# Optimization experiments

Hardware: AMD Instinct MI355X
Metric: run time of the kernel (lower is better)

Reference implementation:

```python
import jax, jax.numpy as jnp
import numpy as np
import math

N_GENES_TOTAL = 5000   # full gene table (fragments.n_genes)
N_CELLS_TOTAL = 10000  # full cell count (libsize buffer)
NBINS = 128            # spline components per gene
N_LATENT = 64
B = 256                # n_cells in minibatch
G = 2000               # genes_oi
NCUTS = 500_000


def setup_inputs() -> dict:
    key = jax.random.key(0)
    ks = jax.random.split(key, 12)
    latent = jax.random.normal(ks[0], (B, N_LATENT), jnp.float32)
    genes_oi = jax.random.randint(ks[1], (G,), 0, N_GENES_TOTAL)
    cells_oi = jax.random.randint(ks[2], (B,), 0, N_CELLS_TOTAL)
    cut_coordinates = jax.random.uniform(ks[3], (NCUTS,), jnp.float32)
    cut_local_cellxgene_ix = jax.random.randint(ks[4], (NCUTS,), 0, B * G)
    cut_local_gene_ix = jax.random.randint(ks[5], (NCUTS,), 0, G)
    local_cellxgene_ix = jax.random.randint(ks[6], (NCUTS,), 0, B * G)
    s = 1.0 / math.sqrt(N_LATENT)
    logit_weight = jax.random.uniform(ks[7], (N_GENES_TOTAL, N_LATENT, NBINS), jnp.float32, -s, s)
    rho_weight = jax.random.uniform(ks[8], (N_GENES_TOTAL, N_LATENT), jnp.float32, -s / 100.0, s / 100.0)
    rho_bias = jax.random.uniform(ks[9], (N_GENES_TOTAL,), jnp.float32, 1e-4, 1e-2)
    libsize = jax.random.randint(ks[10], (N_CELLS_TOTAL,), 1000, 20000)
    spline_heights = 0.01 * jax.random.normal(ks[11], (N_GENES_TOTAL, NBINS), jnp.float32)
    return {
        "latent": latent, "genes_oi": genes_oi, "cells_oi": cells_oi,
        "cut_coordinates": cut_coordinates,
        "cut_local_cellxgene_ix": cut_local_cellxgene_ix,
        "cut_local_gene_ix": cut_local_gene_ix,
        "local_cellxgene_ix": local_cellxgene_ix,
        "logit_weight": logit_weight, "rho_weight": rho_weight,
        "rho_bias": rho_bias, "libsize": libsize,
        "spline_heights": spline_heights,
        "n_cells": B, "n_genes": G,
    }


def reference(latent, genes_oi, cells_oi, cut_coordinates,
              cut_local_cellxgene_ix, cut_local_gene_ix, local_cellxgene_ix,
              logit_weight, rho_weight, rho_bias, libsize, spline_heights,
              n_cells, n_genes):
    # Decoder with n_layers=0: nn is identity
    lw = logit_weight[genes_oi]                     # [G, L, C]
    rw = rho_weight[genes_oi]                       # [G, L]
    mixture_delta = jnp.einsum('bl,glc->bgc', latent, lw)   # [B, G, C]
    rho_delta = latent @ rw.T                       # [B, G]

    # gather per-cut mixture deltas
    delta_flat = mixture_delta.reshape(n_cells * n_genes, -1)
    delta_cut = delta_flat[cut_local_cellxgene_ix]  # [Ncuts, C]

    # spline/mixture log-likelihood: per-gene histogram density with delta
    gene_heights = spline_heights[genes_oi]         # [G, C]
    h = gene_heights[cut_local_gene_ix] + delta_cut  # [Ncuts, C]
    logp_bins = jax.nn.log_softmax(h, axis=-1)
    nbins = h.shape[-1]
    bin_ix = jnp.clip((cut_coordinates * nbins).astype(jnp.int32), 0, nbins - 1)
    likelihood_mixture = (
        jnp.take_along_axis(logp_bins, bin_ix[:, None], axis=-1)[:, 0]
        + jnp.log(jnp.float32(nbins))
    )

    # Poisson fragment-count likelihood
    rate = (rho_bias[genes_oi][None, :] * jnp.exp(rho_delta)
            * libsize[cells_oi].astype(jnp.float32)[:, None])   # [B, G]
    counts = jnp.bincount(local_cellxgene_ix, length=n_cells * n_genes)
    counts = counts.reshape(n_cells, n_genes).astype(jnp.float32)
    ll_counts = counts * jnp.log(rate) - rate - jax.scipy.special.gammaln(counts + 1.0)

    likelihood = likelihood_mixture.sum() + ll_counts.sum()
    return -likelihood
```

## Files before the change

kernel.cpp:

```cpp
#include <hip/hip_runtime.h>

#define LDIM 64
#define CDIM 128
#define NREP 8
#define SUBCAP 48
#define MAXPER (NREP * SUBCAP)
#define LOG128 4.8520302639196171f

typedef __attribute__((ext_vector_type(8))) short bfrag;
typedef __attribute__((ext_vector_type(4))) float f32x4;

static __device__ __forceinline__ unsigned short f2bf(float f) {
    unsigned int x = __float_as_uint(f);
    unsigned int r = (x + 0x7fffu + ((x >> 16) & 1u)) >> 16;
    return (unsigned short)r;
}
static __device__ __forceinline__ float bf2f(unsigned int u) {
    return __uint_as_float(u << 16);
}

__global__ __launch_bounds__(256) void zero_kernel(uint4* __restrict__ p, size_t n16,
                                                   float* __restrict__ out, int out_size) {
    size_t i = (size_t)blockIdx.x * blockDim.x + threadIdx.x;
    size_t stride = (size_t)gridDim.x * blockDim.x;
    for (; i < n16; i += stride) p[i] = make_uint4(0u, 0u, 0u, 0u);
    if (blockIdx.x == 0 && threadIdx.x < (unsigned)out_size) out[threadIdx.x] = 0.f;
}

__global__ __launch_bounds__(256) void prep1_kernel(
    const float* __restrict__ heights, unsigned short* __restrict__ hbf, int nheights,
    const float* __restrict__ latent, unsigned short* __restrict__ latbf, int nlat,
    const int* __restrict__ cut_pair, const int* __restrict__ cut_gene,
    const float* __restrict__ coord, const int* __restrict__ genes_oi,
    const int* __restrict__ local_cxg, unsigned int* __restrict__ cnt_rep,
    unsigned int* __restrict__ bucket, unsigned int* __restrict__ countsT,
    int ncuts, int B, int G, int N, unsigned int magicG) {
    int stride = gridDim.x * blockDim.x;
    int rep = blockIdx.x & (NREP - 1);
    int nb = 2 * G;
    for (int i = blockIdx.x * blockDim.x + threadIdx.x; i < N; i += stride) {
        if (i < nheights) hbf[i] = f2bf(heights[i]);
        if (i < nlat) latbf[i] = f2bf(latent[i]);
        if (i < ncuts) {
            unsigned int p = (unsigned int)cut_pair[i];
            unsigned int cell = __umulhi(p, magicG);
            unsigned int g = p - cell * (unsigned int)G;
            unsigned int gg = (unsigned int)genes_oi[cut_gene[i]];
            int bin = (int)(coord[i] * 128.0f);
            bin = min(max(bin, 0), 127);
            unsigned int bidx = g * 2u + (cell >> 7);
            unsigned int slot = atomicAdd(&cnt_rep[rep * nb + (int)bidx], 1u);
            if (slot < SUBCAP)
                bucket[(size_t)bidx * MAXPER + rep * SUBCAP + slot] =
                    (cell << 24) | (gg << 7) | (unsigned int)bin;
            unsigned int q = (unsigned int)local_cxg[i];
            unsigned int cell2 = __umulhi(q, magicG);
            unsigned int g2 = q - cell2 * (unsigned int)G;
            atomicAdd(&countsT[(size_t)g2 * (unsigned int)B + cell2], 1u);
        }
    }
}

__global__ __launch_bounds__(512, 6) void fused_kernel(
    const float* __restrict__ latent, const unsigned short* __restrict__ latbf,
    const int* __restrict__ genes_oi, const float* __restrict__ logit_weight,
    const unsigned short* __restrict__ hbf, const unsigned int* __restrict__ bucket,
    const unsigned int* __restrict__ cnt_rep, const unsigned int* __restrict__ countsT,
    const int* __restrict__ cells_oi,
    const float* __restrict__ rho_weight, const float* __restrict__ rho_bias,
    const int* __restrict__ libsize, int B, int G, float* __restrict__ out) {
    __shared__ unsigned short dlds[128 * CDIM];
    __shared__ unsigned short blds[CDIM * LDIM];
    __shared__ unsigned int clds[MAXPER];
    __shared__ unsigned int csum[NREP + 1];
    __shared__ float red[8];
    int t = threadIdx.x;
    int bid = blockIdx.x;
    int g = bid >> 1, half = bid & 1;
    int gene = genes_oi[g];
    int nb = 2 * G;

    {
        int n = t & 127;
        int k0 = (t >> 7) * 16;
        const float* src = logit_weight + (size_t)gene * LDIM * CDIM;
        float v[16];
        #pragma unroll
        for (int j = 0; j < 16; ++j) v[j] = src[(size_t)(k0 + j) * CDIM + n];
        #pragma unroll
        for (int h = 0; h < 2; ++h) {
            union { unsigned short u[8]; uint4 q; } pk;
            #pragma unroll
            for (int j = 0; j < 8; ++j) pk.u[j] = f2bf(v[h * 8 + j]);
            int kk = k0 + h * 8;
            *(uint4*)(blds + n * LDIM + (kk ^ ((n & 7) * 8))) = pk.q;
        }
    }
    if (t < NREP) csum[t + 1] = min(cnt_rep[t * nb + bid], (unsigned)SUBCAP);
    __syncthreads();

    int wv = t >> 6, ln = t & 63;
    int l15 = ln & 15, l4 = ln >> 4;
    f32x4 acc[8];
    #pragma unroll
    for (int n = 0; n < 8; ++n) acc[n] = (f32x4){0.f, 0.f, 0.f, 0.f};
    #pragma unroll
    for (int ks = 0; ks < 2; ++ks) {
        int kk = ks * 32 + l4 * 8;
        bfrag a = *(const bfrag*)(latbf + (half * 128 + wv * 16 + l15) * LDIM + kk);
        #pragma unroll
        for (int n = 0; n < 8; ++n) {
            int col = n * 16 + l15;
            bfrag b = *(const bfrag*)(blds + col * LDIM + (kk ^ ((col & 7) * 8)));
            acc[n] = __builtin_amdgcn_mfma_f32_16x16x32_bf16(a, b, acc[n], 0, 0, 0);
        }
    }
    #pragma unroll
    for (int n = 0; n < 8; ++n)
        #pragma unroll
        for (int r = 0; r < 4; ++r) {
            int row = wv * 16 + l4 * 4 + r;
            int col = n * 16 + l15;
            dlds[row * CDIM + (col ^ ((row & 7) * 8))] = f2bf(acc[n][r]);
        }
    if (t == 0) {
        csum[0] = 0;
        #pragma unroll
        for (int r = 0; r < NREP; ++r) csum[r + 1] += csum[r];
    }
    __syncthreads();

    {
        const unsigned int* bk = bucket + (size_t)bid * MAXPER;
        #pragma unroll
        for (int r = 0; r < NREP; ++r) {
            unsigned int base = csum[r], cr = csum[r + 1] - base;
            for (unsigned int i = (unsigned int)t; i < cr; i += 512u)
                clds[base + i] = bk[r * SUBCAP + i];
        }
    }
    __syncthreads();

    float accs = 0.f;
    {
        unsigned int C = csum[NREP];
        int grp = t >> 3, sub = t & 7;
        for (unsigned int i = (unsigned int)grp; i < C; i += 64u) {
            unsigned int rc = clds[i];
            int row = (int)((rc >> 24) & 127u);
            unsigned int gg = (rc >> 7) & 0x1FFFu;
            int sw = (row & 7) * 8;
            uint4 dva = *(const uint4*)(dlds + row * CDIM + ((sub * 16) ^ sw));
            uint4 dvb = *(const uint4*)(dlds + row * CDIM + ((sub * 16 + 8) ^ sw));
            const uint4* hp = (const uint4*)(hbf + ((size_t)gg << 7) + sub * 16);
            uint4 hva = hp[0], hvb = hp[1];
            float h0  = bf2f(hva.x & 0xffffu) + bf2f(dva.x & 0xffffu);
            float h1  = bf2f(hva.x >> 16)     + bf2f(dva.x >> 16);
            float h2  = bf2f(hva.y & 0xffffu) + bf2f(dva.y & 0xffffu);
            float h3  = bf2f(hva.y >> 16)     + bf2f(dva.y >> 16);
            float h4  = bf2f(hva.z & 0xffffu) + bf2f(dva.z & 0xffffu);
            float h5  = bf2f(hva.z >> 16)     + bf2f(dva.z >> 16);
            float h6  = bf2f(hva.w & 0xffffu) + bf2f(dva.w & 0xffffu);
            float h7  = bf2f(hva.w >> 16)     + bf2f(dva.w >> 16);
            float h8  = bf2f(hvb.x & 0xffffu) + bf2f(dvb.x & 0xffffu);
            float h9  = bf2f(hvb.x >> 16)     + bf2f(dvb.x >> 16);
            float h10 = bf2f(hvb.y & 0xffffu) + bf2f(dvb.y & 0xffffu);
            float h11 = bf2f(hvb.y >> 16)     + bf2f(dvb.y >> 16);
            float h12 = bf2f(hvb.z & 0xffffu) + bf2f(dvb.z & 0xffffu);
            float h13 = bf2f(hvb.z >> 16)     + bf2f(dvb.z >> 16);
            float h14 = bf2f(hvb.w & 0xffffu) + bf2f(dvb.w & 0xffffu);
            float h15 = bf2f(hvb.w >> 16)     + bf2f(dvb.w >> 16);
            float s = __expf(h0)  + __expf(h1)  + __expf(h2)  + __expf(h3)
                    + __expf(h4)  + __expf(h5)  + __expf(h6)  + __expf(h7)
                    + __expf(h8)  + __expf(h9)  + __expf(h10) + __expf(h11)
                    + __expf(h12) + __expf(h13) + __expf(h14) + __expf(h15);
            #pragma unroll
            for (int o = 1; o < 8; o <<= 1) s += __shfl_xor(s, o);
            int bin = (int)(rc & 127u);
            int e = bin & 15;
            float sel = h0;
            sel = (e == 1)  ? h1  : sel;
            sel = (e == 2)  ? h2  : sel;
            sel = (e == 3)  ? h3  : sel;
            sel = (e == 4)  ? h4  : sel;
            sel = (e == 5)  ? h5  : sel;
            sel = (e == 6)  ? h6  : sel;
            sel = (e == 7)  ? h7  : sel;
            sel = (e == 8)  ? h8  : sel;
            sel = (e == 9)  ? h9  : sel;
            sel = (e == 10) ? h10 : sel;
            sel = (e == 11) ? h11 : sel;
            sel = (e == 12) ? h12 : sel;
            sel = (e == 13) ? h13 : sel;
            sel = (e == 14) ? h14 : sel;
            sel = (e == 15) ? h15 : sel;
            float hsel = __shfl(sel, (ln & 56) | (bin >> 4));
            if (sub == 0) accs += hsel - __logf(s) + LOG128;
        }
    }

    if (t < 128) {
        int cell = half * 128 + t;
        const float4* la = (const float4*)(latent + (size_t)cell * LDIM);
        const float4* rw = (const float4*)(rho_weight + (size_t)gene * LDIM);
        float d = 0.f;
        #pragma unroll
        for (int k = 0; k < LDIM / 4; ++k) {
            float4 a = la[k], w = rw[k];
            d += a.x * w.x + a.y * w.y + a.z * w.z + a.w * w.w;
        }
        float rb = rho_bias[gene];
        float lib = (float)libsize[cells_oi[cell]];
        float lrate = __logf(rb) + d + __logf(lib);
        float rate = __expf(lrate);
        unsigned int c = countsT[(size_t)g * B + cell];
        float lgam = 0.f;
        for (unsigned int k = 2; k <= c; ++k) lgam += __logf((float)k);
        accs += (float)c * lrate - rate - lgam;
    }

    #pragma unroll
    for (int o = 32; o; o >>= 1) accs += __shfl_xor(accs, o);
    if (ln == 0) red[wv] = accs;
    __syncthreads();
    if (t == 0) {
        float s = red[0] + red[1] + red[2] + red[3] + red[4] + red[5] + red[6] + red[7];
        atomicAdd(out, -s);
    }
}

extern "C" void kernel_launch(void* const* d_in, const int* in_sizes, int n_in,
                              void* d_out, int out_size, void* d_ws, size_t ws_size,
                              hipStream_t stream) {
    const float* latent         = (const float*)d_in[0];
    const int*   genes_oi       = (const int*)d_in[1];
    const int*   cells_oi       = (const int*)d_in[2];
    const float* cut_coord      = (const float*)d_in[3];
    const int*   cut_pair       = (const int*)d_in[4];
    const int*   cut_gene       = (const int*)d_in[5];
    const int*   local_cxg      = (const int*)d_in[6];
    const float* logit_weight   = (const float*)d_in[7];
    const float* rho_weight     = (const float*)d_in[8];
    const float* rho_bias       = (const float*)d_in[9];
    const int*   libsize        = (const int*)d_in[10];
    const float* spline_heights = (const float*)d_in[11];
    int G = in_sizes[1];
    int B = in_sizes[2];
    int ncuts = in_sizes[4];
    int nheights = in_sizes[11];
    int nlat = B * LDIM;
    unsigned int magicG = (unsigned int)((0x100000000ULL + (unsigned)G - 1) / (unsigned)G);

    char* ws = (char*)d_ws;
    size_t off = 0;
    unsigned int* countsT = (unsigned int*)(ws + off);
    off += ((size_t)B * G * 4 + 255) & ~(size_t)255;
    unsigned int* cnt_rep = (unsigned int*)(ws + off);
    off += ((size_t)2 * G * NREP * 4 + 255) & ~(size_t)255;
    size_t zero_bytes = off;
    unsigned int* bucket = (unsigned int*)(ws + off);
    off += ((size_t)2 * G * MAXPER * 4 + 255) & ~(size_t)255;
    unsigned short* hbf = (unsigned short*)(ws + off);
    off += ((size_t)nheights * 2 + 255) & ~(size_t)255;
    unsigned short* latbf = (unsigned short*)(ws + off);
    off += ((size_t)nlat * 2 + 255) & ~(size_t)255;

    float* out = (float*)d_out;
    zero_kernel<<<1024, 256, 0, stream>>>((uint4*)ws, zero_bytes / 16, out, out_size);

    int N = ncuts > nheights ? ncuts : nheights;
    prep1_kernel<<<2048, 256, 0, stream>>>(
        spline_heights, hbf, nheights, latent, latbf, nlat,
        cut_pair, cut_gene, cut_coord, genes_oi, local_cxg,
        cnt_rep, bucket, countsT, ncuts, B, G, N, magicG);
    fused_kernel<<<2 * G, 512, 0, stream>>>(
        latent, latbf, genes_oi, logit_weight, hbf, bucket,
        cnt_rep, countsT, cells_oi,
        rho_weight, rho_bias, libsize, B, G, out);
}
```

Measured before the change: 139.3 us.

## Hoist loads and bucket copy before first barrier, drop shared prefix sum

Issues the global loads (logit weights, latent A fragments, bucket counts) at kernel entry. Each thread now computes the bucket prefix sum in registers, so the shared csum array goes away. The bucket-to-LDS copy and the Poisson count term move ahead of the first barrier, which removes one __syncthreads and lets these memory latencies overlap. The replica count also changes from 8×48 to 16×32 slots, which doubles the per-thread cnt_rep reads and changes how cuts are spread across replicas. This assumes the bucketing kernel in the unseen part of the code uses the same NREP and SUBCAP macros.

Measured after the change: 144.9 us. +4.0%, slower.

```diff
diff --git a/kernel.cpp b/kernel.cpp
--- a/kernel.cpp
+++ b/kernel.cpp
@@ -2,8 +2,8 @@
 
 #define LDIM 64
 #define CDIM 128
-#define NREP 8
-#define SUBCAP 48
+#define NREP 16
+#define SUBCAP 32
 #define MAXPER (NREP * SUBCAP)
 #define LOG128 4.8520302639196171f
 
@@ -72,78 +72,100 @@
     __shared__ unsigned short dlds[128 * CDIM];
     __shared__ unsigned short blds[CDIM * LDIM];
     __shared__ unsigned int clds[MAXPER];
-    __shared__ unsigned int csum[NREP + 1];
     __shared__ float red[8];
     int t = threadIdx.x;
     int bid = blockIdx.x;
     int g = bid >> 1, half = bid & 1;
     int gene = genes_oi[g];
     int nb = 2 * G;
+    int wv = t >> 6, ln = t & 63;
+    int l15 = ln & 15, l4 = ln >> 4;
+    float accs = 0.f;
+
+    int n = t & 127;
+    int k0 = (t >> 7) * 16;
+    const float* src = logit_weight + (size_t)gene * LDIM * CDIM;
+    float wv_[16];
+    #pragma unroll
+    for (int j = 0; j < 16; ++j) wv_[j] = src[(size_t)(k0 + j) * CDIM + n];
+    bfrag a_[2];
+    #pragma unroll
+    for (int ks = 0; ks < 2; ++ks)
+        a_[ks] = *(const bfrag*)(latbf + (half * 128 + wv * 16 + l15) * LDIM + ks * 32 + l4 * 8);
+
+    unsigned int cs[NREP + 1];
+    cs[0] = 0;
+    #pragma unroll
+    for (int r = 0; r < NREP; ++r)
+        cs[r + 1] = cs[r] + min(cnt_rep[r * nb + bid], (unsigned)SUBCAP);
+
+    if (t < 128) {
+        int cell = half * 128 + t;
+        const float4* la = (const float4*)(latent + (size_t)cell * LDIM);
+        const float4* rw = (const float4*)(rho_weight + (size_t)gene * LDIM);
+        float d = 0.f;
+        #pragma unroll
+        for (int k = 0; k < LDIM / 4; ++k) {
+            float4 a = la[k], w = rw[k];
+            d += a.x * w.x + a.y * w.y + a.z * w.z + a.w * w.w;
+        }
+        float rb = rho_bias[gene];
+        float lib = (float)libsize[cells_oi[cell]];
+        float lrate = __logf(rb) + d + __logf(lib);
+        float rate = __expf(lrate);
+        unsigned int c = countsT[(size_t)g * B + cell];
+        float lgam = 0.f;
+        for (unsigned int k = 2; k <= c; ++k) lgam += __logf((float)k);
+        accs += (float)c * lrate - rate - lgam;
+    }
 
     {
-        int n = t & 127;
-        int k0 = (t >> 7) * 16;
-        const float* src = logit_weight + (size_t)gene * LDIM * CDIM;
-        float v[16];
-        #pragma unroll
-        for (int j = 0; j < 16; ++j) v[j] = src[(size_t)(k0 + j) * CDIM + n];
+        const unsigned int* bk = bucket + (size_t)bid * MAXPER;
+        #pragma unroll
+        for (int r = 0; r < NREP; ++r) {
+            unsigned int base = cs[r], cr = cs[r + 1] - base;
+            for (unsigned int i = (unsigned int)t; i < cr; i += 512u)
+                clds[base + i] = bk[r * SUBCAP + i];
+        }
+    }
+
+    {
         #pragma unroll
         for (int h = 0; h < 2; ++h) {
             union { unsigned short u[8]; uint4 q; } pk;
             #pragma unroll
-            for (int j = 0; j < 8; ++j) pk.u[j] = f2bf(v[h * 8 + j]);
+            for (int j = 0; j < 8; ++j) pk.u[j] = f2bf(wv_[h * 8 + j]);
             int kk = k0 + h * 8;
             *(uint4*)(blds + n * LDIM + (kk ^ ((n & 7) * 8))) = pk.q;
         }
     }
-    if (t < NREP) csum[t + 1] = min(cnt_rep[t * nb + bid], (unsigned)SUBCAP);
     __syncthreads();
 
-    int wv = t >> 6, ln = t & 63;
-    int l15 = ln & 15, l4 = ln >> 4;
     f32x4 acc[8];
     #pragma unroll
-    for (int n = 0; n < 8; ++n) acc[n] = (f32x4){0.f, 0.f, 0.f, 0.f};
+    for (int q = 0; q < 8; ++q) acc[q] = (f32x4){0.f, 0.f, 0.f, 0.f};
     #pragma unroll
     for (int ks = 0; ks < 2; ++ks) {
         int kk = ks * 32 + l4 * 8;
-        bfrag a = *(const bfrag*)(latbf + (half * 128 + wv * 16 + l15) * LDIM + kk);
-        #pragma unroll
-        for (int n = 0; n < 8; ++n) {
-            int col = n * 16 + l15;
+        #pragma unroll
+        for (int q = 0; q < 8; ++q) {
+            int col = q * 16 + l15;
             bfrag b = *(const bfrag*)(blds + col * LDIM + (kk ^ ((col & 7) * 8)));
-            acc[n] = __builtin_amdgcn_mfma_f32_16x16x32_bf16(a, b, acc[n], 0, 0, 0);
-        }
-    }
-    #pragma unroll
-    for (int n = 0; n < 8; ++n)
+            acc[q] = __builtin_amdgcn_mfma_f32_16x16x32_bf16(a_[ks], b, acc[q], 0, 0, 0);
+        }
+    }
+    #pragma unroll
+    for (int q = 0; q < 8; ++q)
         #pragma unroll
         for (int r = 0; r < 4; ++r) {
             int row = wv * 16 + l4 * 4 + r;
-            int col = n * 16 + l15;
-            dlds[row * CDIM + (col ^ ((row & 7) * 8))] = f2bf(acc[n][r]);
-        }
-    if (t == 0) {
-        csum[0] = 0;
-        #pragma unroll
-        for (int r = 0; r < NREP; ++r) csum[r + 1] += csum[r];
-    }
+            int col = q * 16 + l15;
+            dlds[row * CDIM + (col ^ ((row & 7) * 8))] = f2bf(acc[q][r]);
+        }
     __syncthreads();
 
     {
-        const unsigned int* bk = bucket + (size_t)bid * MAXPER;
-        #pragma unroll
-        for (int r = 0; r < NREP; ++r) {
-            unsigned int base = csum[r], cr = csum[r + 1] - base;
-            for (unsigned int i = (unsigned int)t; i < cr; i += 512u)
-                clds[base + i] = bk[r * SUBCAP + i];
-        }
-    }
-    __syncthreads();
-
-    float accs = 0.f;
-    {
-        unsigned int C = csum[NREP];
+        unsigned int C = cs[NREP];
         int grp = t >> 3, sub = t & 7;
         for (unsigned int i = (unsigned int)grp; i < C; i += 64u) {
             unsigned int rc = clds[i];
@@ -199,26 +221,6 @@
         }
     }
 
-    if (t < 128) {
-        int cell = half * 128 + t;
-        const float4* la = (const float4*)(latent + (size_t)cell * LDIM);
-        const float4* rw = (const float4*)(rho_weight + (size_t)gene * LDIM);
-        float d = 0.f;
-        #pragma unroll
-        for (int k = 0; k < LDIM / 4; ++k) {
-            float4 a = la[k], w = rw[k];
-            d += a.x * w.x + a.y * w.y + a.z * w.z + a.w * w.w;
-        }
-        float rb = rho_bias[gene];
-        float lib = (float)libsize[cells_oi[cell]];
-        float lrate = __logf(rb) + d + __logf(lib);
-        float rate = __expf(lrate);
-        unsigned int c = countsT[(size_t)g * B + cell];
-        float lgam = 0.f;
-        for (unsigned int k = 2; k <= c; ++k) lgam += __logf((float)k);
-        accs += (float)c * lrate - rate - lgam;
-    }
-
     #pragma unroll
     for (int o = 32; o; o >>= 1) accs += __shfl_xor(accs, o);
     if (ln == 0) red[wv] = accs;
```
